# Kernel optimization log

Hardware: AMD Instinct MI355X
Metric: run time of the kernel (lower is better)

The kernel has to match this reference:

```python
import jax, jax.numpy as jnp
import numpy as np

FS = 128; WIN = 4; C_IN = 64; C_OUT = 512; BATCH = 1024
K = FS // 4            # conv kernel = 32
STRIDE = K // 2        # 16
WS = FS * WIN          # 512 samples
T = (WS - K) // STRIDE + 1  # 31 time steps
THRESH = 1.0
BN_EPS = 1e-5

# snntorch-style spike with ATan surrogate (alpha=2): fwd Heaviside, bwd 1/(1+(pi*x)^2)
@jax.custom_vjp
def spike_fn(x):
    return (x > 0).astype(x.dtype)

def _spike_fwd(x):
    return (x > 0).astype(x.dtype), x

def _spike_bwd(x, g):
    return (g / (1.0 + (jnp.pi * x) ** 2),)

spike_fn.defvjp(_spike_fwd, _spike_bwd)

def leaky_step(inp, mem, beta):
    # snntorch Leaky, reset_mechanism='subtract': reset computed from PREVIOUS mem, detached
    reset = jax.lax.stop_gradient((mem > THRESH).astype(mem.dtype))
    mem_new = jnp.clip(beta, 0.0, 1.0) * mem + inp - reset * THRESH
    spk = spike_fn(mem_new - THRESH)
    return spk, mem_new

def setup_inputs() -> dict:
    key = jax.random.key(0)
    ks = jax.random.split(key, 10)
    return {
        "x": jax.random.normal(ks[0], (BATCH, C_IN, WS), jnp.float32),
        "conv_w": jax.random.normal(ks[1], (C_OUT, C_IN, K), jnp.float32) * (1.0 / np.sqrt(C_IN * K)),
        "conv_b": jax.random.normal(ks[2], (C_OUT,), jnp.float32) * 0.01,
        "bn_gamma": jnp.ones((C_OUT,), jnp.float32),
        "bn_beta": jnp.zeros((C_OUT,), jnp.float32),
        "bn_mean": jnp.zeros((C_OUT,), jnp.float32),
        "bn_var": jnp.ones((C_OUT,), jnp.float32),
        "fc1_w": jax.random.normal(ks[3], (C_OUT, C_OUT), jnp.float32) * (1.0 / np.sqrt(C_OUT)),
        "fc1_b": jax.random.normal(ks[4], (C_OUT,), jnp.float32) * 0.01,
        "fc2_w": jax.random.normal(ks[5], (2, C_OUT), jnp.float32) * (1.0 / np.sqrt(C_OUT)),
        "fc2_b": jax.random.normal(ks[6], (2,), jnp.float32) * 0.01,
        "beta_enc": jax.random.uniform(ks[7], (C_OUT,), jnp.float32),
        "beta_hid": jax.random.uniform(ks[8], (C_OUT,), jnp.float32),
        "beta_out": jax.random.uniform(ks[9], (2,), jnp.float32),
    }

def reference(x, conv_w, conv_b, bn_gamma, bn_beta, bn_mean, bn_var,
              fc1_w, fc1_b, fc2_w, fc2_b, beta_enc, beta_hid, beta_out):
    # Conv1d: x [B, C_in, WS] -> [B, C_out, T]
    out = jax.lax.conv_general_dilated(
        x, conv_w, window_strides=(STRIDE,), padding='VALID',
        dimension_numbers=('NCH', 'OIH', 'NCH')) + conv_b[None, :, None]
    # BatchNorm1d (eval mode with running stats); dropout is identity in eval
    inv = jax.lax.rsqrt(bn_var + BN_EPS)
    out = bn_gamma[None, :, None] * (out - bn_mean[None, :, None]) * inv[None, :, None] + bn_beta[None, :, None]
    seq = jnp.transpose(out, (2, 0, 1))  # [T, B, C_out]

    mems0 = (jnp.zeros((BATCH, C_OUT), out.dtype),
             jnp.zeros((BATCH, C_OUT), out.dtype),
             jnp.zeros((BATCH, 2), out.dtype))

    def step(carry, xt):
        em, hm, om = carry
        spk_e, em = leaky_step(xt, em, beta_enc)
        cur1 = spk_e @ fc1_w.T + fc1_b
        spk_h, hm = leaky_step(cur1, hm, beta_hid)
        cur2 = spk_h @ fc2_w.T + fc2_b
        spk_o, om = leaky_step(cur2, om, beta_out)
        return (em, hm, om), (spk_o, om)

    (em, hm, om), (spk_rec, mem_rec) = jax.lax.scan(step, mems0, seq)
    return om, spk_rec, mem_rec
```

## Files before the change

### kernel.cpp

```cpp
#include <hip/hip_runtime.h>

#define T_STEPS 31
#define CIN     64
#define COUT    512
#define WSLEN   512
#define CSTRIDE 16
#define KRED    2048
#define NBATCH  1024
#define BCHUNK  512
#define MCHUNK  (BCHUNK * T_STEPS)
#define NMT     (MCHUNK / 16)
#define XPLANE  16777216

typedef int v4i __attribute__((ext_vector_type(4)));

__device__ __forceinline__ double clip01d(double v) { return fmin(fmax(v, 0.0), 1.0); }

__device__ __forceinline__ void gl_lds16(const void* g, void* l) {
    __builtin_amdgcn_global_load_lds(
        (const __attribute__((address_space(1))) void*)g,
        (__attribute__((address_space(3))) void*)l, 16, 0, 0);
}

__device__ __forceinline__ void dig5(float4 f, unsigned int w[5]) {
    float vv[4] = {f.x, f.y, f.z, f.w};
    unsigned int w0 = 0, w1 = 0, w2 = 0, w3 = 0, w4 = 0;
    #pragma unroll
    for (int e = 0; e < 4; ++e) {
        float v  = vv[e];
        float c0 = rintf(v * 16384.0f);
        float r1 = fmaf(c0, -6.103515625e-05f, v);
        float c1 = rintf(r1 * 268435456.0f);
        float r2 = fmaf(c1, -3.725290298461914e-09f, r1);
        float c2 = rintf(r2 * 34359738368.0f);
        int i0 = (int)c0, i1 = (int)c1, i2 = (int)c2;
        int d2 = ((i0 + 64) & 127) - 64;
        int d1 = (i0 - d2) >> 7;
        int d4 = ((i1 + 64) & 127) - 64;
        int d3 = (i1 - d4) >> 7;
        w0 |= (unsigned int)(d1 & 255) << (8 * e);
        w1 |= (unsigned int)(d2 & 255) << (8 * e);
        w2 |= (unsigned int)(d3 & 255) << (8 * e);
        w3 |= (unsigned int)(d4 & 255) << (8 * e);
        w4 |= (unsigned int)(i2 & 255) << (8 * e);
    }
    w[0] = w0; w[1] = w1; w[2] = w2; w[3] = w3; w[4] = w4;
}

__global__ __launch_bounds__(256) void prep_digits_kernel(
    const float* __restrict__ conv_w, const float* __restrict__ fc1_w,
    signed char* __restrict__ Bd, signed char* __restrict__ Fd)
{
    int t = blockIdx.x * 256 + threadIdx.x;
    if (t < 262144) {
        int k4 = (t & 511) << 2;
        int co = t >> 9;
        float4 w4 = *(const float4*)(conv_w + (size_t)co * KRED + k4);
        float4 v4 = make_float4(w4.x * 4.0f, w4.y * 4.0f, w4.z * 4.0f, w4.w * 4.0f);
        unsigned int pk[5];
        dig5(v4, pk);
        int off = (((k4 >> 6) * 32 + (co >> 4)) << 10)
                + ((co & 15) + ((k4 >> 4) & 3) * 16) * 16 + (k4 & 15);
        #pragma unroll
        for (int q = 0; q < 5; ++q)
            *(unsigned int*)(Bd + q * 1048576 + off) = pk[q];
    } else {
        int u  = t - 262144;
        int k4 = (u & 127) << 2;
        int co = u >> 7;
        float4 w4 = *(const float4*)(fc1_w + (size_t)co * COUT + k4);
        float4 v4 = make_float4(w4.x * 4.0f, w4.y * 4.0f, w4.z * 4.0f, w4.w * 4.0f);
        unsigned int pk[5];
        dig5(v4, pk);
        int off = (((k4 >> 6) * 32 + (co >> 4)) << 10)
                + ((co & 15) + ((k4 >> 4) & 3) * 16) * 16 + (k4 & 15);
        #pragma unroll
        for (int q = 0; q < 5; ++q)
            *(unsigned int*)(Fd + q * 262144 + off) = pk[q];
    }
}

__global__ __launch_bounds__(256) void digx_kernel(
    const float* __restrict__ x, signed char* __restrict__ Xd, int b_base)
{
    size_t t = (size_t)blockIdx.x * 256 + threadIdx.x;
    size_t off4 = t * 4;
    float4 v = *(const float4*)(x + (size_t)b_base * CIN * WSLEN + off4);
    unsigned int pk[5];
    dig5(make_float4(v.x * 0.125f, v.y * 0.125f, v.z * 0.125f, v.w * 0.125f), pk);
    #pragma unroll
    for (int p = 0; p < 5; ++p)
        *(unsigned int*)(Xd + (size_t)p * XPLANE + off4) = pk[p];
}

__global__ __launch_bounds__(512) void conv_bn_i8v11_kernel(
    const signed char* __restrict__ Xd, const signed char* __restrict__ Bd,
    const float* __restrict__ conv_b,
    const float* __restrict__ bn_gamma, const float* __restrict__ bn_beta,
    const float* __restrict__ bn_mean,  const float* __restrict__ bn_var,
    double* __restrict__ seq)
{
    __shared__ __align__(16) signed char Alds[5 * 2048];
    __shared__ __align__(16) signed char Blds[5 * 8192];

    const int tid = threadIdx.x;
    const int nMB = MCHUNK / 32;
    const int bm  = blockIdx.x % nMB;
    const int bnk = blockIdx.x / nMB;
    const int m0 = bm * 32, n0 = bnk * 128;

    const int wv  = tid >> 6;
    const int l   = tid & 63;
    const int rgM = wv >> 2;
    const int cw  = wv & 3;

    const int rL = l & 15, qL = l >> 4;
    const int st0 = wv & 1;
    const int m_0 = m0 + st0 * 16 + rL;
    const int bl0 = m_0 / T_STEPS, t_0 = m_0 % T_STEPS;
    const signed char* srcA0 = Xd + (size_t)(wv >> 1) * XPLANE
        + ((size_t)(bl0 * 64 + (qL >> 1)) << 9) + t_0 * 16 + (qL & 1) * 16;
    signed char* dstA0 = Alds + (wv >> 1) * 2048 + st0 * 1024;
    const int m_1 = m0 + (wv & 1) * 16 + rL;
    const int bl1 = m_1 / T_STEPS, t_1 = m_1 % T_STEPS;
    const signed char* srcA1 = Xd + (size_t)4 * XPLANE
        + ((size_t)(bl1 * 64 + (qL >> 1)) << 9) + t_1 * 16 + (qL & 1) * 16;
    signed char* dstA1 = Alds + 4 * 2048 + (wv & 1) * 1024;

    v4i acc[2][5];
    #pragma unroll
    for (int s = 0; s < 2; ++s)
        #pragma unroll
        for (int d = 0; d < 5; ++d) acc[s][d] = (v4i){0, 0, 0, 0};

    for (int kt = 0; kt < 32; ++kt) {
        __syncthreads();

        gl_lds16(srcA0 + kt * 1024, dstA0);
        if (wv < 2) gl_lds16(srcA1 + kt * 1024, dstA1);

        #pragma unroll
        for (int i = 0; i < 5; ++i) {
            const int s   = wv * 5 + i;
            const int q   = s >> 3;
            const int ctl = s & 7;
            const signed char* gsrc = Bd + (size_t)q * 1048576
                + (((size_t)(kt * 32 + bnk * 8 + ctl)) << 10) + l * 16;
            gl_lds16(gsrc, Blds + q * 8192 + ctl * 1024);
        }
        __syncthreads();

        v4i aF[5];
        #pragma unroll
        for (int p = 0; p < 5; ++p)
            aF[p] = *(const v4i*)(Alds + p * 2048 + (rgM << 10) + (l << 4));

        #define MF(A_, B_, C_) __builtin_amdgcn_mfma_i32_16x16x64_i8(A_, B_, C_, 0, 0, 0)
        #pragma unroll
        for (int s = 0; s < 2; ++s) {
            const signed char* bb = Blds + ((cw * 2 + s) << 10) + (l << 4);
            v4i b0 = *(const v4i*)(bb);
            v4i b1 = *(const v4i*)(bb + 8192);
            v4i b2 = *(const v4i*)(bb + 16384);
            v4i b3 = *(const v4i*)(bb + 24576);
            v4i b4 = *(const v4i*)(bb + 32768);
            acc[s][0] = MF(aF[0], b0, acc[s][0]);
            acc[s][1] = MF(aF[1], b0, MF(aF[0], b1, acc[s][1]));
            acc[s][2] = MF(aF[2], b0, MF(aF[1], b1, MF(aF[0], b2, acc[s][2])));
            acc[s][3] = MF(aF[3], b0, MF(aF[2], b1, MF(aF[1], b2, MF(aF[0], b3, acc[s][3]))));
            acc[s][4] = MF(aF[4], b0, MF(aF[3], b1, MF(aF[2], b2, MF(aF[1], b3, MF(aF[0], b4, acc[s][4])))));
        }
        #undef MF
    }

    const int l15 = l & 15;
    const int rq  = l >> 4;
    #pragma unroll
    for (int s = 0; s < 2; ++s) {
        const int co = n0 + (cw * 2 + s) * 16 + l15;
        const double g   = (double)bn_gamma[co];
        const double be  = (double)bn_beta[co];
        const double mn  = (double)bn_mean[co];
        const double vr  = (double)bn_var[co];
        const double cb  = (double)conv_b[co];
        const double inv = 1.0 / sqrt(vr + 1e-5);
        #pragma unroll
        for (int r = 0; r < 4; ++r) {
            double v = (double)acc[s][0][r] * 0x1p-13
                     + (double)acc[s][1][r] * 0x1p-20
                     + (double)acc[s][2][r] * 0x1p-27
                     + (double)acc[s][3][r] * 0x1p-34
                     + (double)acc[s][4][r] * 0x1p-41;
            int m = m0 + rgM * 16 + rq * 4 + r;
            seq[(size_t)m * COUT + co] = g * (v + cb - mn) * inv + be;
        }
    }
}

__global__ __launch_bounds__(512) void conv_bn_i8v6_kernel(
    const float* __restrict__ x, const signed char* __restrict__ Bd,
    const float* __restrict__ conv_b,
    const float* __restrict__ bn_gamma, const float* __restrict__ bn_beta,
    const float* __restrict__ bn_mean,  const float* __restrict__ bn_var,
    double* __restrict__ seq, int b_base)
{
    __shared__ __align__(16) signed char Alds[5 * 2048];
    __shared__ __align__(16) signed char Blds[5 * 8192];

    const int tid = threadIdx.x;
    const int nMB = MCHUNK / 32;
    const int bm  = blockIdx.x % nMB;
    const int bnk = blockIdx.x / nMB;
    const int m0 = bm * 32, n0 = bnk * 128;

    const int rA  = tid & 31;
    const int gA  = tid >> 5;
    const int kqA = gA & 3;
    const int jq  = gA >> 2;
    const int mA  = m0 + rA;
    const int bA  = b_base + mA / T_STEPS;
    const int tA  = mA % T_STEPS;
    const float* xp = x + (size_t)bA * CIN * WSLEN + tA * CSTRIDE;
    const int awb  = ((rA >> 4) << 10) + ((rA & 15) + kqA * 16) * 16 + jq * 4;
    const int kloc = kqA * 16 + jq * 4;

    const int wv  = tid >> 6;
    const int l   = tid & 63;
    const int rgM = wv >> 2;
    const int cw  = wv & 3;

    v4i acc[2][5];
    #pragma unroll
    for (int s = 0; s < 2; ++s)
        #pragma unroll
        for (int d = 0; d < 5; ++d) acc[s][d] = (v4i){0, 0, 0, 0};

    float4 sxa = *(const float4*)(xp + (kloc >> 5) * WSLEN + (kloc & 31));

    for (int kt = 0; kt < 32; ++kt) {
        unsigned int pa[5];
        dig5(make_float4(sxa.x * 0.125f, sxa.y * 0.125f, sxa.z * 0.125f, sxa.w * 0.125f), pa);

        __syncthreads();
        #pragma unroll
        for (int p = 0; p < 5; ++p)
            *(unsigned int*)(Alds + p * 2048 + awb) = pa[p];

        #pragma unroll
        for (int i = 0; i < 5; ++i) {
            const int s   = wv * 5 + i;
            const int q   = s >> 3;
            const int ctl = s & 7;
            const signed char* gsrc = Bd + (size_t)q * 1048576
                + (((size_t)(kt * 32 + bnk * 8 + ctl)) << 10) + l * 16;
            gl_lds16(gsrc, Blds + q * 8192 + ctl * 1024);
        }

        if (kt + 1 < 32) {
            int gk = (kt + 1) * 64 + kloc;
            sxa = *(const float4*)(xp + (gk >> 5) * WSLEN + (gk & 31));
        }
        __syncthreads();

        v4i aF[5];
        #pragma unroll
        for (int p = 0; p < 5; ++p)
            aF[p] = *(const v4i*)(Alds + p * 2048 + (rgM << 10) + (l << 4));

        #define MF(A_, B_, C_) __builtin_amdgcn_mfma_i32_16x16x64_i8(A_, B_, C_, 0, 0, 0)
        #pragma unroll
        for (int s = 0; s < 2; ++s) {
            const signed char* bb = Blds + ((cw * 2 + s) << 10) + (l << 4);
            v4i b0 = *(const v4i*)(bb);
            v4i b1 = *(const v4i*)(bb + 8192);
            v4i b2 = *(const v4i*)(bb + 16384);
            v4i b3 = *(const v4i*)(bb + 24576);
            v4i b4 = *(const v4i*)(bb + 32768);
            acc[s][0] = MF(aF[0], b0, acc[s][0]);
            acc[s][1] = MF(aF[1], b0, MF(aF[0], b1, acc[s][1]));
            acc[s][2] = MF(aF[2], b0, MF(aF[1], b1, MF(aF[0], b2, acc[s][2])));
            acc[s][3] = MF(aF[3], b0, MF(aF[2], b1, MF(aF[1], b2, MF(aF[0], b3, acc[s][3]))));
            acc[s][4] = MF(aF[4], b0, MF(aF[3], b1, MF(aF[2], b2, MF(aF[1], b3, MF(aF[0], b4, acc[s][4])))));
        }
        #undef MF
    }

    const int l15 = l & 15;
    const int rq  = l >> 4;
    #pragma unroll
    for (int s = 0; s < 2; ++s) {
        const int co = n0 + (cw * 2 + s) * 16 + l15;
        const double g   = (double)bn_gamma[co];
        const double be  = (double)bn_beta[co];
        const double mn  = (double)bn_mean[co];
        const double vr  = (double)bn_var[co];
        const double cb  = (double)conv_b[co];
        const double inv = 1.0 / sqrt(vr + 1e-5);
        #pragma unroll
        for (int r = 0; r < 4; ++r) {
            double v = (double)acc[s][0][r] * 0x1p-13
                     + (double)acc[s][1][r] * 0x1p-20
                     + (double)acc[s][2][r] * 0x1p-27
                     + (double)acc[s][3][r] * 0x1p-34
                     + (double)acc[s][4][r] * 0x1p-41;
            int m = m0 + rgM * 16 + rq * 4 + r;
            seq[(size_t)m * COUT + co] = g * (v + cb - mn) * inv + be;
        }
    }
}

__global__ __launch_bounds__(512) void enc_scan_kernel(
    const double* __restrict__ seq, const float* __restrict__ beta_enc,
    signed char* __restrict__ Sd)
{
    const int c = threadIdx.x;
    const int b = blockIdx.x;
    const double be = clip01d((double)beta_enc[c]);
    const double* sp = seq + (size_t)b * T_STEPS * COUT + c;
    const size_t cblk = (size_t)(c >> 6) * NMT;
    const int    coff = ((c >> 4) & 3) * 16;
    const int    j    = c & 15;
    double em = 0.0;
    for (int t = 0; t < T_STEPS; ++t) {
        double e = be * em + sp[(size_t)t * COUT] - ((em > 1.0) ? 1.0 : 0.0);
        em = e;
        int m = b * T_STEPS + t;
        Sd[((cblk + (m >> 4)) << 10) + ((m & 15) + coff) * 16 + j] =
            (e > 1.0) ? (signed char)1 : (signed char)0;
    }
}

__global__ __launch_bounds__(512) void fc1_gemm_kernel(
    const signed char* __restrict__ Sd, const signed char* __restrict__ Fd,
    double* __restrict__ cur1)
{
    __shared__ __align__(16) signed char AldsK[2048];
    __shared__ __align__(16) signed char BldsK[5 * 8192];

    const int tid = threadIdx.x;
    const int nMB = MCHUNK / 32;
    const int bm  = blockIdx.x % nMB;
    const int bnk = blockIdx.x / nMB;
    const int m0 = bm * 32, n0 = bnk * 128;

    const int wv  = tid >> 6;
    const int l   = tid & 63;
    const int rgM = wv >> 2;
    const int cw  = wv & 3;

    v4i acc[2][5];
    #pragma unroll
    for (int s = 0; s < 2; ++s)
        #pragma unroll
        for (int d = 0; d < 5; ++d) acc[s][d] = (v4i){0, 0, 0, 0};

    for (int kt = 0; kt < 8; ++kt) {
        __syncthreads();
        #pragma unroll
        for (int i = 0; i < 5; ++i) {
            const int s   = wv * 5 + i;
            const int q   = s >> 3;
            const int ctl = s & 7;
            const signed char* gsrc = Fd + (size_t)q * 262144
                + (((size_t)(kt * 32 + bnk * 8 + ctl)) << 10) + l * 16;
            gl_lds16(gsrc, BldsK + q * 8192 + ctl * 1024);
        }
        if (wv < 2) {
            const signed char* gsrc = Sd
                + (((size_t)(kt * NMT + bm * 2 + wv)) << 10) + l * 16;
            gl_lds16(gsrc, AldsK + wv * 1024);
        }
        __syncthreads();

        v4i aF = *(const v4i*)(AldsK + (rgM << 10) + (l << 4));
        #define MF(A_, B_, C_) __builtin_amdgcn_mfma_i32_16x16x64_i8(A_, B_, C_, 0, 0, 0)
        #pragma unroll
        for (int s = 0; s < 2; ++s) {
            const signed char* bb = BldsK + ((cw * 2 + s) << 10) + (l << 4);
            acc[s][0] = MF(aF, *(const v4i*)(bb),         acc[s][0]);
            acc[s][1] = MF(aF, *(const v4i*)(bb + 8192),  acc[s][1]);
            acc[s][2] = MF(aF, *(const v4i*)(bb + 16384), acc[s][2]);
            acc[s][3] = MF(aF, *(const v4i*)(bb + 24576), acc[s][3]);
            acc[s][4] = MF(aF, *(const v4i*)(bb + 32768), acc[s][4]);
        }
        #undef MF
    }

    const int l15 = l & 15;
    const int rq  = l >> 4;
    #pragma unroll
    for (int s = 0; s < 2; ++s) {
        const int co = n0 + (cw * 2 + s) * 16 + l15;
        #pragma unroll
        for (int r = 0; r < 4; ++r) {
            double v = (double)acc[s][0][r] * 0x1p-9
                     + (double)acc[s][1][r] * 0x1p-16
                     + (double)acc[s][2][r] * 0x1p-23
                     + (double)acc[s][3][r] * 0x1p-30
                     + (double)acc[s][4][r] * 0x1p-37;
            int m = m0 + rgM * 16 + rq * 4 + r;
            cur1[(size_t)m * COUT + co] = v;
        }
    }
}

__global__ __launch_bounds__(512, 4) void hid_out_scan_kernel(
    const double* __restrict__ cur1, const float* __restrict__ fc1_b,
    const float* __restrict__ fc2_w, const float* __restrict__ fc2_b,
    const float* __restrict__ beta_hid, const float* __restrict__ beta_out,
    float* __restrict__ out, int b_base)
{
    __shared__ double red[8][2];

    const int tid  = threadIdx.x;
    const int lane = tid & 63;
    const int wave = tid >> 6;
    const int row  = blockIdx.x;
    const int brow = b_base + row;

    const double bh  = clip01d((double)beta_hid[tid]);
    const double f1b = (double)fc1_b[tid];
    const double w2a = (double)fc2_w[tid];
    const double w2b = (double)fc2_w[COUT + tid];

    double bo = 0.0, f2b = 0.0, om = 0.0;
    if (tid < 2) { bo = clip01d((double)beta_out[tid]); f2b = (double)fc2_b[tid]; }

    double hm = 0.0;
    const double* cp = cur1 + (size_t)row * T_STEPS * COUT + tid;

    for (int t = 0; t < T_STEPS; ++t) {
        double cur = cp[(size_t)t * COUT] + f1b;
        double h = bh * hm + cur - ((hm > 1.0) ? 1.0 : 0.0);
        hm = h;
        double sh = (h > 1.0) ? 1.0 : 0.0;
        double p0 = sh * w2a;
        double p1 = sh * w2b;
        #pragma unroll
        for (int off = 32; off > 0; off >>= 1) {
            p0 += __shfl_down(p0, off);
            p1 += __shfl_down(p1, off);
        }
        if (lane == 0) { red[wave][0] = p0; red[wave][1] = p1; }
        __syncthreads();
        if (tid < 2) {
            double cur2 = f2b;
            #pragma unroll
            for (int w = 0; w < 8; ++w) cur2 += red[w][tid];
            double o = bo * om + cur2 - ((om > 1.0) ? 1.0 : 0.0);
            om = o;
            float so = (o > 1.0) ? 1.0f : 0.0f;
            int bidx = brow * 2 + tid;
            out[2048 + t * 2048 + bidx] = so;
            out[2048 + 63488 + t * 2048 + bidx] = (float)o;
            if (t == T_STEPS - 1) out[bidx] = (float)o;
        }
        __syncthreads();
    }
}

extern "C" void kernel_launch(void* const* d_in, const int* in_sizes, int n_in,
                              void* d_out, int out_size, void* d_ws, size_t ws_size,
                              hipStream_t stream)
{
    const float* x        = (const float*)d_in[0];
    const float* conv_w   = (const float*)d_in[1];
    const float* conv_b   = (const float*)d_in[2];
    const float* bn_gamma = (const float*)d_in[3];
    const float* bn_beta  = (const float*)d_in[4];
    const float* bn_mean  = (const float*)d_in[5];
    const float* bn_var   = (const float*)d_in[6];
    const float* fc1_w    = (const float*)d_in[7];
    const float* fc1_b    = (const float*)d_in[8];
    const float* fc2_w    = (const float*)d_in[9];
    const float* fc2_b    = (const float*)d_in[10];
    const float* beta_enc = (const float*)d_in[11];
    const float* beta_hid = (const float*)d_in[12];
    const float* beta_out = (const float*)d_in[13];
    float* out = (float*)d_out;

    signed char* Bd  = (signed char*)d_ws;
    signed char* Fd  = (signed char*)d_ws + 5 * 1048576;
    signed char* Sd  = (signed char*)d_ws + 7 * 1048576;
    double*      seq = (double*)((char*)d_ws + 16 * 1048576);

    prep_digits_kernel<<<1280, 256, 0, stream>>>(conv_w, fc1_w, Bd, Fd);

    const size_t NEED_XD = 160ull * 1048576;
    if (ws_size >= NEED_XD) {
        signed char* Xd = (signed char*)d_ws + 80ull * 1048576;
        for (int chunk = 0; chunk < 2; ++chunk) {
            int b_base = chunk * BCHUNK;
            digx_kernel<<<16384, 256, 0, stream>>>(x, Xd, b_base);
            conv_bn_i8v11_kernel<<<(MCHUNK / 32) * (COUT / 128), 512, 0, stream>>>(
                Xd, Bd, conv_b, bn_gamma, bn_beta, bn_mean, bn_var, seq);
            enc_scan_kernel<<<BCHUNK, 512, 0, stream>>>(seq, beta_enc, Sd);
            fc1_gemm_kernel<<<(MCHUNK / 32) * (COUT / 128), 512, 0, stream>>>(
                Sd, Fd, seq);
            hid_out_scan_kernel<<<BCHUNK, 512, 0, stream>>>(
                seq, fc1_b, fc2_w, fc2_b, beta_hid, beta_out, out, b_base);
        }
    } else {
        for (int chunk = 0; chunk < 2; ++chunk) {
            int b_base = chunk * BCHUNK;
            conv_bn_i8v6_kernel<<<(MCHUNK / 32) * (COUT / 128), 512, 0, stream>>>(
                x, Bd, conv_b, bn_gamma, bn_beta, bn_mean, bn_var, seq, b_base);
            enc_scan_kernel<<<BCHUNK, 512, 0, stream>>>(seq, beta_enc, Sd);
            fc1_gemm_kernel<<<(MCHUNK / 32) * (COUT / 128), 512, 0, stream>>>(
                Sd, Fd, seq);
            hid_out_scan_kernel<<<BCHUNK, 512, 0, stream>>>(
                seq, fc1_b, fc2_w, fc2_b, beta_hid, beta_out, out, b_base);
        }
    }
}
```

Baseline: 662.3 us.

## Double-buffer LDS in int8 conv GEMM and halve the N tile to 64

The conv GEMM kernel now keeps two LDS buffers and issues the global-to-LDS loads for the next K tile while MFMAs run on the current one. This drops one of the two barriers per iteration. The output-channel tile shrinks from 128 to 64, so each wave holds one accumulator set instead of two and the grid doubles. In exchange, LDS use rises, A tiles are loaded twice as often across blocks, and there is less MFMA work per load to hide latency.

New measurement: 727.7 us. 9.9% more time.

```diff
diff --git a/kernel.cpp b/kernel.cpp
--- a/kernel.cpp
+++ b/kernel.cpp
@@ -93,26 +93,26 @@
         *(unsigned int*)(Xd + (size_t)p * XPLANE + off4) = pk[p];
 }
 
-__global__ __launch_bounds__(512) void conv_bn_i8v11_kernel(
+__global__ __launch_bounds__(512) void conv_bn_i8v12_kernel(
     const signed char* __restrict__ Xd, const signed char* __restrict__ Bd,
     const float* __restrict__ conv_b,
     const float* __restrict__ bn_gamma, const float* __restrict__ bn_beta,
     const float* __restrict__ bn_mean,  const float* __restrict__ bn_var,
     double* __restrict__ seq)
 {
-    __shared__ __align__(16) signed char Alds[5 * 2048];
-    __shared__ __align__(16) signed char Blds[5 * 8192];
+    __shared__ __align__(16) signed char Abuf[2][10240];
+    __shared__ __align__(16) signed char Bbuf[2][20480];
 
     const int tid = threadIdx.x;
     const int nMB = MCHUNK / 32;
     const int bm  = blockIdx.x % nMB;
     const int bnk = blockIdx.x / nMB;
-    const int m0 = bm * 32, n0 = bnk * 128;
+    const int m0 = bm * 32, n0 = bnk * 64;
 
     const int wv  = tid >> 6;
     const int l   = tid & 63;
     const int rgM = wv >> 2;
-    const int cw  = wv & 3;
+    const int cwv = wv & 3;
 
     const int rL = l & 15, qL = l >> 4;
     const int st0 = wv & 1;
@@ -120,64 +120,76 @@
     const int bl0 = m_0 / T_STEPS, t_0 = m_0 % T_STEPS;
     const signed char* srcA0 = Xd + (size_t)(wv >> 1) * XPLANE
         + ((size_t)(bl0 * 64 + (qL >> 1)) << 9) + t_0 * 16 + (qL & 1) * 16;
-    signed char* dstA0 = Alds + (wv >> 1) * 2048 + st0 * 1024;
+    const int offA0 = (wv >> 1) * 2048 + st0 * 1024;
     const int m_1 = m0 + (wv & 1) * 16 + rL;
     const int bl1 = m_1 / T_STEPS, t_1 = m_1 % T_STEPS;
     const signed char* srcA1 = Xd + (size_t)4 * XPLANE
         + ((size_t)(bl1 * 64 + (qL >> 1)) << 9) + t_1 * 16 + (qL & 1) * 16;
-    signed char* dstA1 = Alds + 4 * 2048 + (wv & 1) * 1024;
-
-    v4i acc[2][5];
-    #pragma unroll
-    for (int s = 0; s < 2; ++s)
-        #pragma unroll
-        for (int d = 0; d < 5; ++d) acc[s][d] = (v4i){0, 0, 0, 0};
+    const int offA1 = 4 * 2048 + (wv & 1) * 1024;
+
+    const int sB0 = wv,      qB0 = sB0 >> 2, cB0 = sB0 & 3;
+    const int sB1 = wv + 8,  qB1 = sB1 >> 2, cB1 = sB1 & 3;
+    const int sB2 = wv + 16, qB2 = sB2 >> 2, cB2 = sB2 & 3;
+    const signed char* srcB0 = Bd + (size_t)qB0 * 1048576
+        + (((size_t)(bnk * 4 + cB0)) << 10) + l * 16;
+    const signed char* srcB1 = Bd + (size_t)qB1 * 1048576
+        + (((size_t)(bnk * 4 + cB1)) << 10) + l * 16;
+    const signed char* srcB2 = Bd + (size_t)qB2 * 1048576
+        + (((size_t)(bnk * 4 + cB2)) << 10) + l * 16;
+    const int offB0 = qB0 * 4096 + cB0 * 1024;
+    const int offB1 = qB1 * 4096 + cB1 * 1024;
+    const int offB2 = qB2 * 4096 + cB2 * 1024;
+
+    v4i acc[5];
+    #pragma unroll
+    for (int d = 0; d < 5; ++d) acc[d] = (v4i){0, 0, 0, 0};
+
+    {
+        gl_lds16(srcA0, &Abuf[0][offA0]);
+        if (wv < 2) gl_lds16(srcA1, &Abuf[0][offA1]);
+        gl_lds16(srcB0, &Bbuf[0][offB0]);
+        gl_lds16(srcB1, &Bbuf[0][offB1]);
+        if (wv < 4) gl_lds16(srcB2, &Bbuf[0][offB2]);
+    }
+    __syncthreads();
 
     for (int kt = 0; kt < 32; ++kt) {
-        __syncthreads();
-
-        gl_lds16(srcA0 + kt * 1024, dstA0);
-        if (wv < 2) gl_lds16(srcA1 + kt * 1024, dstA1);
-
-        #pragma unroll
-        for (int i = 0; i < 5; ++i) {
-            const int s   = wv * 5 + i;
-            const int q   = s >> 3;
-            const int ctl = s & 7;
-            const signed char* gsrc = Bd + (size_t)q * 1048576
-                + (((size_t)(kt * 32 + bnk * 8 + ctl)) << 10) + l * 16;
-            gl_lds16(gsrc, Blds + q * 8192 + ctl * 1024);
-        }
-        __syncthreads();
-
-        v4i aF[5];
+        const int cur = kt & 1;
+        const int nxt = cur ^ 1;
+
+        if (kt + 1 < 32) {
+            const size_t koA = (size_t)(kt + 1) * 1024;
+            const size_t koB = (size_t)(kt + 1) * 32768;
+            gl_lds16(srcA0 + koA, &Abuf[nxt][offA0]);
+            if (wv < 2) gl_lds16(srcA1 + koA, &Abuf[nxt][offA1]);
+            gl_lds16(srcB0 + koB, &Bbuf[nxt][offB0]);
+            gl_lds16(srcB1 + koB, &Bbuf[nxt][offB1]);
+            if (wv < 4) gl_lds16(srcB2 + koB, &Bbuf[nxt][offB2]);
+        }
+
+        v4i aF[5], bF[5];
         #pragma unroll
         for (int p = 0; p < 5; ++p)
-            aF[p] = *(const v4i*)(Alds + p * 2048 + (rgM << 10) + (l << 4));
+            aF[p] = *(const v4i*)(&Abuf[cur][p * 2048 + (rgM << 10) + (l << 4)]);
+        #pragma unroll
+        for (int q = 0; q < 5; ++q)
+            bF[q] = *(const v4i*)(&Bbuf[cur][q * 4096 + (cwv << 10) + (l << 4)]);
 
         #define MF(A_, B_, C_) __builtin_amdgcn_mfma_i32_16x16x64_i8(A_, B_, C_, 0, 0, 0)
-        #pragma unroll
-        for (int s = 0; s < 2; ++s) {
-            const signed char* bb = Blds + ((cw * 2 + s) << 10) + (l << 4);
-            v4i b0 = *(const v4i*)(bb);
-            v4i b1 = *(const v4i*)(bb + 8192);
-            v4i b2 = *(const v4i*)(bb + 16384);
-            v4i b3 = *(const v4i*)(bb + 24576);
-            v4i b4 = *(const v4i*)(bb + 32768);
-            acc[s][0] = MF(aF[0], b0, acc[s][0]);
-            acc[s][1] = MF(aF[1], b0, MF(aF[0], b1, acc[s][1]));
-            acc[s][2] = MF(aF[2], b0, MF(aF[1], b1, MF(aF[0], b2, acc[s][2])));
-            acc[s][3] = MF(aF[3], b0, MF(aF[2], b1, MF(aF[1], b2, MF(aF[0], b3, acc[s][3]))));
-            acc[s][4] = MF(aF[4], b0, MF(aF[3], b1, MF(aF[2], b2, MF(aF[1], b3, MF(aF[0], b4, acc[s][4])))));
-        }
+        acc[0] = MF(aF[0], bF[0], acc[0]);
+        acc[1] = MF(aF[1], bF[0], MF(aF[0], bF[1], acc[1]));
+        acc[2] = MF(aF[2], bF[0], MF(aF[1], bF[1], MF(aF[0], bF[2], acc[2])));
+        acc[3] = MF(aF[3], bF[0], MF(aF[2], bF[1], MF(aF[1], bF[2], MF(aF[0], bF[3], acc[3]))));
+        acc[4] = MF(aF[4], bF[0], MF(aF[3], bF[1], MF(aF[2], bF[2], MF(aF[1], bF[3], MF(aF[0], bF[4], acc[4])))));
         #undef MF
+
+        __syncthreads();
     }
 
     const int l15 = l & 15;
     const int rq  = l >> 4;
-    #pragma unroll
-    for (int s = 0; s < 2; ++s) {
-        const int co = n0 + (cw * 2 + s) * 16 + l15;
+    {
+        const int co = n0 + cwv * 16 + l15;
         const double g   = (double)bn_gamma[co];
         const double be  = (double)bn_beta[co];
         const double mn  = (double)bn_mean[co];
@@ -186,11 +198,11 @@
         const double inv = 1.0 / sqrt(vr + 1e-5);
         #pragma unroll
         for (int r = 0; r < 4; ++r) {
-            double v = (double)acc[s][0][r] * 0x1p-13
-                     + (double)acc[s][1][r] * 0x1p-20
-                     + (double)acc[s][2][r] * 0x1p-27
-                     + (double)acc[s][3][r] * 0x1p-34
-                     + (double)acc[s][4][r] * 0x1p-41;
+            double v = (double)acc[0][r] * 0x1p-13
+                     + (double)acc[1][r] * 0x1p-20
+                     + (double)acc[2][r] * 0x1p-27
+                     + (double)acc[3][r] * 0x1p-34
+                     + (double)acc[4][r] * 0x1p-41;
             int m = m0 + rgM * 16 + rq * 4 + r;
             seq[(size_t)m * COUT + co] = g * (v + cb - mn) * inv + be;
         }
@@ -492,7 +504,7 @@
         for (int chunk = 0; chunk < 2; ++chunk) {
             int b_base = chunk * BCHUNK;
             digx_kernel<<<16384, 256, 0, stream>>>(x, Xd, b_base);
-            conv_bn_i8v11_kernel<<<(MCHUNK / 32) * (COUT / 128), 512, 0, stream>>>(
+            conv_bn_i8v12_kernel<<<(MCHUNK / 32) * (COUT / 64), 512, 0, stream>>>(
                 Xd, Bd, conv_b, bn_gamma, bn_beta, bn_mean, bn_var, seq);
             enc_scan_kernel<<<BCHUNK, 512, 0, stream>>>(seq, beta_enc, Sd);
             fc1_gemm_kernel<<<(MCHUNK / 32) * (COUT / 128), 512, 0, stream>>>(
```
